# Kernel optimization log

Measured on AMD Instinct MI355X. Metric: run time of the kernel, lower is better.

## Reference

```python
import jax, jax.numpy as jnp
import numpy as np

EMBED = 1024
HIDDEN = 512
LN_EPS = 1e-5


def setup_inputs() -> dict:
    key = jax.random.key(0)
    ks = jax.random.split(key, 9)
    B, Sq, Skv = 4, 4096, 4096
    q_feat = jax.random.normal(ks[0], (B, Sq, EMBED), dtype=jnp.float32)
    kv_feat = jax.random.normal(ks[1], (B, Skv, EMBED), dtype=jnp.float32)
    # xavier-ish scale for weights; stored as [in, out]
    def w(k, fan_in, fan_out):
        s = (6.0 / (fan_in + fan_out)) ** 0.5
        return jax.random.uniform(k, (fan_in, fan_out), jnp.float32, -s, s)
    Wq = w(ks[2], EMBED, HIDDEN)
    Wk = w(ks[3], EMBED, HIDDEN)
    Wv = w(ks[4], EMBED, HIDDEN)
    Wo = w(ks[5], HIDDEN, EMBED)
    bo = jnp.zeros((EMBED,), jnp.float32)
    Wfc = w(ks[6], EMBED, EMBED)
    ln_gamma = jnp.ones((EMBED,), jnp.float32)
    ln_beta = jnp.zeros((EMBED,), jnp.float32)
    return {"q_feat": q_feat, "kv_feat": kv_feat, "Wq": Wq, "Wk": Wk, "Wv": Wv,
            "Wo": Wo, "bo": bo, "Wfc": Wfc, "ln_gamma": ln_gamma, "ln_beta": ln_beta}


def reference(q_feat, kv_feat, Wq, Wk, Wv, Wo, bo, Wfc, ln_gamma, ln_beta):
    # projections (single head)
    Q = jnp.einsum('bse,eh->bsh', q_feat, Wq)
    K = jnp.einsum('bse,eh->bsh', kv_feat, Wk)
    V = jnp.einsum('bse,eh->bsh', kv_feat, Wv)
    scale = 1.0 / jnp.sqrt(jnp.asarray(HIDDEN, Q.dtype))
    scores = jnp.einsum('bqh,bkh->bqk', Q, K) * scale  # [B, Sq, Skv]
    attn = jax.nn.softmax(scores, axis=-1)
    ctx = jnp.einsum('bqk,bkh->bqh', attn, V)
    out = jnp.einsum('bqh,he->bqe', ctx, Wo) + bo
    out = out + q_feat  # residual
    out = jnp.einsum('bqe,ef->bqf', out, Wfc)
    # layer norm over last dim
    mu = jnp.mean(out, axis=-1, keepdims=True)
    var = jnp.mean(jnp.square(out - mu), axis=-1, keepdims=True)
    out = (out - mu) * jax.lax.rsqrt(var + LN_EPS) * ln_gamma + ln_beta
    return out
```

## Files before the change

kernel.cpp:

```cpp
#include <hip/hip_runtime.h>
#include <hip/hip_bf16.h>
#include <cstdint>

typedef __bf16 bf16x8 __attribute__((ext_vector_type(8)));
typedef float f32x4 __attribute__((ext_vector_type(4)));
typedef unsigned short u16;
typedef unsigned short u16x8 __attribute__((ext_vector_type(8)));
typedef unsigned short u16x4 __attribute__((ext_vector_type(4)));

#define EMBED 1024
#define HIDDEN 512
#define SEQ 4096
#define NBATCH 4
#define MTOT (NBATCH * SEQ)
#define KVSPLIT 2

__device__ __forceinline__ u16 f32_to_bf16(float f) {
  union { float f; uint32_t u; } v; v.f = f;
  uint32_t r = v.u + 0x7fffu + ((v.u >> 16) & 1u);
  return (u16)(r >> 16);
}

__device__ __forceinline__ void load_lds16(const u16* g, u16* l) {
  __builtin_amdgcn_global_load_lds(
      (const __attribute__((address_space(1))) void*)g,
      (__attribute__((address_space(3))) void*)l, 16, 0, 0);
}

__global__ __launch_bounds__(256) void cvt_bf16_kernel(const float* __restrict__ src,
                                                       u16* __restrict__ dst) {
  int i = blockIdx.x * 256 + threadIdx.x;
  float4 v = ((const float4*)src)[i];
  u16x4 o;
  o[0] = f32_to_bf16(v.x); o[1] = f32_to_bf16(v.y);
  o[2] = f32_to_bf16(v.z); o[3] = f32_to_bf16(v.w);
  ((u16x4*)dst)[i] = o;
}

__global__ __launch_bounds__(256) void transpose_w_kernel(const float* __restrict__ src,
                                                          u16* __restrict__ dst,
                                                          int log2N, int K) {
  int idx = blockIdx.x * 256 + threadIdx.x;
  int N = 1 << log2N;
  int k = idx >> log2N;
  int n = idx & (N - 1);
  dst[(size_t)n * K + k] = f32_to_bf16(src[idx]);
}

template <int MODE>
__global__ __launch_bounds__(256, 3) void gemm_bt_kernel(
    const u16* __restrict__ A, const u16* __restrict__ Bt, void* __restrict__ Cout,
    const float* __restrict__ bias, const float* __restrict__ resid,
    int ldc, int K, float scale) {
  __shared__ u16 As[128][40];
  __shared__ u16 Bs[128][40];
  const int tid = threadIdx.x;
  const int lane = tid & 63;
  const int wave = tid >> 6;
  const int quad = lane >> 4;
  const int l15 = lane & 15;
  const int m0 = blockIdx.x * 128;
  const int n0 = blockIdx.y * 128;
  const int wm = (wave & 1) * 64;
  const int wn = (wave >> 1) * 64;

  f32x4 acc[4][4];
#pragma unroll
  for (int i = 0; i < 4; ++i)
#pragma unroll
    for (int j = 0; j < 4; ++j) {
      acc[i][j][0] = 0.f; acc[i][j][1] = 0.f; acc[i][j][2] = 0.f; acc[i][j][3] = 0.f;
    }

  for (int k0 = 0; k0 < K; k0 += 32) {
    __syncthreads();
#pragma unroll
    for (int p = 0; p < 2; ++p) {
      int c = tid + p * 256;
      int r = c >> 2;
      int c8 = (c & 3) * 8;
      *(u16x8*)&As[r][c8] = *(const u16x8*)&A[(size_t)(m0 + r) * K + k0 + c8];
      *(u16x8*)&Bs[r][c8] = *(const u16x8*)&Bt[(size_t)(n0 + r) * K + k0 + c8];
    }
    __syncthreads();
    bf16x8 af[4], bfr[4];
#pragma unroll
    for (int i = 0; i < 4; ++i) af[i] = *(const bf16x8*)&As[wm + i * 16 + l15][quad * 8];
#pragma unroll
    for (int j = 0; j < 4; ++j) bfr[j] = *(const bf16x8*)&Bs[wn + j * 16 + l15][quad * 8];
#pragma unroll
    for (int i = 0; i < 4; ++i)
#pragma unroll
      for (int j = 0; j < 4; ++j)
        acc[i][j] = __builtin_amdgcn_mfma_f32_16x16x32_bf16(af[i], bfr[j], acc[i][j], 0, 0, 0);
  }

#pragma unroll
  for (int i = 0; i < 4; ++i) {
    const int row = m0 + wm + i * 16 + quad * 4;
#pragma unroll
    for (int j = 0; j < 4; ++j) {
      const int col = n0 + wn + j * 16 + l15;
#pragma unroll
      for (int r = 0; r < 4; ++r) {
        float v = acc[i][j][r];
        const int rr = row + r;
        if (MODE == 0) {
          ((u16*)Cout)[(size_t)rr * ldc + col] = f32_to_bf16(v * scale);
        } else if (MODE == 1) {
          const size_t off = (size_t)rr * ldc + col;
          v += bias[col] + resid[off];
          ((u16*)Cout)[off] = f32_to_bf16(v);
        } else if (MODE == 2) {
          ((float*)Cout)[(size_t)rr * ldc + col] = v;
        } else {
          ((u16*)Cout)[((size_t)((rr >> 12) * 512 + col) << 12) + (rr & 4095)] = f32_to_bf16(v);
        }
      }
    }
  }
}

__global__ __launch_bounds__(256, 2) void flash_kernel(const u16* __restrict__ QKV,
                                                       const u16* __restrict__ VtG,
                                                       float* __restrict__ Opart,
                                                       float* __restrict__ ml) {
  __shared__ u16 Ks[32][520];
  __shared__ u16 Vs[512][32];
  __shared__ u16 Ps[4][16][40];
  const int tid = threadIdx.x;
  const int lane = tid & 63;
  const int wave = tid >> 6;
  const int quad = lane >> 4;
  const int l15 = lane & 15;
  const int base = blockIdx.y * SEQ;
  const int b512 = blockIdx.y * 512;
  const int q0 = blockIdx.x * 64;
  const int kvb = blockIdx.z * (SEQ / KVSPLIT);

  bf16x8 qf[16];
  {
    const u16* qp = QKV + (size_t)(base + q0 + wave * 16 + l15) * 1024 + quad * 8;
#pragma unroll
    for (int ks = 0; ks < 16; ++ks) qf[ks] = *(const bf16x8*)(qp + ks * 32);
  }

  f32x4 O[32];
#pragma unroll
  for (int i = 0; i < 32; ++i) { O[i][0] = 0.f; O[i][1] = 0.f; O[i][2] = 0.f; O[i][3] = 0.f; }
  float m_run[4] = {-INFINITY, -INFINITY, -INFINITY, -INFINITY};
  float l_run[4] = {0.f, 0.f, 0.f, 0.f};

  for (int kv0 = kvb; kv0 < kvb + SEQ / KVSPLIT; kv0 += 32) {
    __syncthreads();
    {
      const int rk = wave * 8;
      const u16* kp = QKV + (size_t)(base + kv0 + rk) * 1024 + 512 + lane * 8;
      const u16* vp = VtG + (size_t)(b512 + wave * 128 + (lane >> 2)) * 4096 + kv0 +
                      (((lane & 3) ^ ((lane >> 3) & 3)) * 8);
#pragma unroll
      for (int p = 0; p < 8; ++p) {
        load_lds16(kp + (size_t)p * 1024, &Ks[rk + p][0]);
        load_lds16(vp + (size_t)(p * 16) * 4096, &Vs[wave * 128 + p * 16][0]);
      }
    }
    __syncthreads();

    f32x4 s0, s1;
    s0[0] = 0.f; s0[1] = 0.f; s0[2] = 0.f; s0[3] = 0.f;
    s1[0] = 0.f; s1[1] = 0.f; s1[2] = 0.f; s1[3] = 0.f;
#pragma unroll
    for (int ks = 0; ks < 16; ++ks) {
      bf16x8 b0 = *(const bf16x8*)&Ks[l15][ks * 32 + quad * 8];
      bf16x8 b1 = *(const bf16x8*)&Ks[16 + l15][ks * 32 + quad * 8];
      s0 = __builtin_amdgcn_mfma_f32_16x16x32_bf16(qf[ks], b0, s0, 0, 0, 0);
      s1 = __builtin_amdgcn_mfma_f32_16x16x32_bf16(qf[ks], b1, s1, 0, 0, 0);
    }

    float tmax[4], alpha[4], p0[4], p1[4], tsum[4];
#pragma unroll
    for (int r = 0; r < 4; ++r) tmax[r] = fmaxf(s0[r], s1[r]);
#pragma unroll
    for (int m = 1; m <= 8; m <<= 1)
#pragma unroll
      for (int r = 0; r < 4; ++r) tmax[r] = fmaxf(tmax[r], __shfl_xor(tmax[r], m));
    bool aone = true;
#pragma unroll
    for (int r = 0; r < 4; ++r) {
      float mnew = fmaxf(m_run[r], tmax[r]);
      alpha[r] = __expf(m_run[r] - mnew);
      m_run[r] = mnew;
      p0[r] = __expf(s0[r] - mnew);
      p1[r] = __expf(s1[r] - mnew);
      tsum[r] = p0[r] + p1[r];
      aone = aone && (alpha[r] == 1.0f);
    }
#pragma unroll
    for (int m = 1; m <= 8; m <<= 1)
#pragma unroll
      for (int r = 0; r < 4; ++r) tsum[r] += __shfl_xor(tsum[r], m);
#pragma unroll
    for (int r = 0; r < 4; ++r) l_run[r] = l_run[r] * alpha[r] + tsum[r];
    if (!__all(aone)) {
#pragma unroll
      for (int i = 0; i < 32; ++i)
#pragma unroll
        for (int r = 0; r < 4; ++r) O[i][r] *= alpha[r];
    }

#pragma unroll
    for (int r = 0; r < 4; ++r) {
      Ps[wave][quad * 4 + r][l15] = f32_to_bf16(p0[r]);
      Ps[wave][quad * 4 + r][16 + l15] = f32_to_bf16(p1[r]);
    }
    asm volatile("s_waitcnt lgkmcnt(0)" ::: "memory");
    bf16x8 pf = *(const bf16x8*)&Ps[wave][l15][quad * 8];
#pragma unroll
    for (int nt = 0; nt < 32; ++nt) {
      bf16x8 vf = *(const bf16x8*)&Vs[nt * 16 + l15][(quad ^ ((l15 >> 1) & 3)) * 8];
      O[nt] = __builtin_amdgcn_mfma_f32_16x16x32_bf16(pf, vf, O[nt], 0, 0, 0);
    }
  }

  const int qrow = base + q0 + wave * 16 + quad * 4;
  float* op = Opart + ((size_t)blockIdx.z * MTOT + qrow) * HIDDEN;
#pragma unroll
  for (int nt = 0; nt < 32; ++nt)
#pragma unroll
    for (int r = 0; r < 4; ++r)
      op[(size_t)r * HIDDEN + nt * 16 + l15] = O[nt][r];
  if (l15 == 0) {
#pragma unroll
    for (int r = 0; r < 4; ++r) {
      ml[((size_t)blockIdx.z * MTOT + qrow + r) * 2 + 0] = m_run[r];
      ml[((size_t)blockIdx.z * MTOT + qrow + r) * 2 + 1] = l_run[r];
    }
  }
}

__global__ __launch_bounds__(128) void combine_kernel(const float* __restrict__ Op,
                                                      const float* __restrict__ ml,
                                                      u16* __restrict__ ctx) {
  const int row = blockIdx.x;
  const int tid = threadIdx.x;
  const float m1 = ml[(size_t)row * 2], l1 = ml[(size_t)row * 2 + 1];
  const float m2 = ml[((size_t)MTOT + row) * 2], l2 = ml[((size_t)MTOT + row) * 2 + 1];
  const float M = fmaxf(m1, m2);
  const float w1 = __expf(m1 - M), w2 = __expf(m2 - M);
  const float den = 1.0f / (w1 * l1 + w2 * l2);
  float4 a = ((const float4*)(Op + (size_t)row * HIDDEN))[tid];
  float4 b = ((const float4*)(Op + ((size_t)MTOT + row) * HIDDEN))[tid];
  u16x4 o;
  o[0] = f32_to_bf16((a.x * w1 + b.x * w2) * den);
  o[1] = f32_to_bf16((a.y * w1 + b.y * w2) * den);
  o[2] = f32_to_bf16((a.z * w1 + b.z * w2) * den);
  o[3] = f32_to_bf16((a.w * w1 + b.w * w2) * den);
  ((u16x4*)(ctx + (size_t)row * HIDDEN))[tid] = o;
}

__global__ __launch_bounds__(256) void ln_kernel(float* __restrict__ io,
                                                 const float* __restrict__ g,
                                                 const float* __restrict__ b) {
  const int row = blockIdx.x;
  const int tid = threadIdx.x;
  float* x = io + (size_t)row * EMBED;
  float4 v = *(const float4*)(x + tid * 4);
  float s1 = v.x + v.y + v.z + v.w;
  float s2 = v.x * v.x + v.y * v.y + v.z * v.z + v.w * v.w;
#pragma unroll
  for (int m = 1; m <= 32; m <<= 1) {
    s1 += __shfl_xor(s1, m);
    s2 += __shfl_xor(s2, m);
  }
  __shared__ float rs1[4], rs2[4];
  const int wave = tid >> 6;
  if ((tid & 63) == 0) { rs1[wave] = s1; rs2[wave] = s2; }
  __syncthreads();
  s1 = rs1[0] + rs1[1] + rs1[2] + rs1[3];
  s2 = rs2[0] + rs2[1] + rs2[2] + rs2[3];
  const float mu = s1 * (1.f / EMBED);
  const float var = s2 * (1.f / EMBED) - mu * mu;
  const float rinv = rsqrtf(var + 1e-5f);
  float4 gg = *(const float4*)(g + tid * 4);
  float4 bb = *(const float4*)(b + tid * 4);
  float4 o;
  o.x = (v.x - mu) * rinv * gg.x + bb.x;
  o.y = (v.y - mu) * rinv * gg.y + bb.y;
  o.z = (v.z - mu) * rinv * gg.z + bb.z;
  o.w = (v.w - mu) * rinv * gg.w + bb.w;
  *(float4*)(x + tid * 4) = o;
}

extern "C" void kernel_launch(void* const* d_in, const int* in_sizes, int n_in,
                              void* d_out, int out_size, void* d_ws, size_t ws_size,
                              hipStream_t stream) {
  const float* q_feat = (const float*)d_in[0];
  const float* kv_feat = (const float*)d_in[1];
  const float* Wq = (const float*)d_in[2];
  const float* Wk = (const float*)d_in[3];
  const float* Wv = (const float*)d_in[4];
  const float* Wo = (const float*)d_in[5];
  const float* bo = (const float*)d_in[6];
  const float* Wfc = (const float*)d_in[7];
  const float* ln_g = (const float*)d_in[8];
  const float* ln_b = (const float*)d_in[9];
  float* out = (float*)d_out;

  char* ws = (char*)d_ws;
  u16* Aq    = (u16*)(ws + 0);
  u16* Akv   = (u16*)(ws + 33554432);
  u16* Wcat  = (u16*)(ws + 67108864);
  u16* Wo_t  = (u16*)(ws + 70254592);
  u16* Wfc_t = (u16*)(ws + 71303168);
  u16* QKV   = (u16*)(ws + 73400320);
  u16* Vt    = (u16*)(ws + 106954752);
  u16* ctx   = (u16*)(ws + 123731968);
  u16* out1  = Aq;
  float* Opart = (float*)(ws + 0);
  float* mlp   = (float*)(ws + 67108864);

  const float qscale = 0.044194173824159216f;

  cvt_bf16_kernel<<<MTOT * EMBED / 1024, 256, 0, stream>>>(q_feat, Aq);
  cvt_bf16_kernel<<<MTOT * EMBED / 1024, 256, 0, stream>>>(kv_feat, Akv);
  transpose_w_kernel<<<(EMBED * HIDDEN) / 256, 256, 0, stream>>>(Wq, Wcat, 9, EMBED);
  transpose_w_kernel<<<(EMBED * HIDDEN) / 256, 256, 0, stream>>>(Wk, Wcat + 512 * 1024, 9, EMBED);
  transpose_w_kernel<<<(EMBED * HIDDEN) / 256, 256, 0, stream>>>(Wv, Wcat + 1024 * 1024, 9, EMBED);
  transpose_w_kernel<<<(HIDDEN * EMBED) / 256, 256, 0, stream>>>(Wo, Wo_t, 10, HIDDEN);
  transpose_w_kernel<<<(EMBED * EMBED) / 256, 256, 0, stream>>>(Wfc, Wfc_t, 10, EMBED);
  gemm_bt_kernel<0><<<dim3(MTOT / 128, 4), 256, 0, stream>>>(
      Aq, Wcat, QKV, nullptr, nullptr, 1024, EMBED, qscale);
  gemm_bt_kernel<0><<<dim3(MTOT / 128, 4), 256, 0, stream>>>(
      Akv, Wcat + 512 * 1024, QKV + 512, nullptr, nullptr, 1024, EMBED, 1.0f);
  gemm_bt_kernel<3><<<dim3(MTOT / 128, 4), 256, 0, stream>>>(
      Akv, Wcat + 1024 * 1024, Vt, nullptr, nullptr, 0, EMBED, 1.0f);
  flash_kernel<<<dim3(SEQ / 64, NBATCH, KVSPLIT), 256, 0, stream>>>(QKV, Vt, Opart, mlp);
  combine_kernel<<<MTOT, 128, 0, stream>>>(Opart, mlp, ctx);
  gemm_bt_kernel<1><<<dim3(MTOT / 128, EMBED / 128), 256, 0, stream>>>(
      ctx, Wo_t, out1, bo, q_feat, EMBED, HIDDEN, 0.f);
  gemm_bt_kernel<2><<<dim3(MTOT / 128, EMBED / 128), 256, 0, stream>>>(
      out1, Wfc_t, out, nullptr, nullptr, EMBED, EMBED, 0.f);
  ln_kernel<<<MTOT, 256, 0, stream>>>(out, ln_g, ln_b);

  (void)in_sizes; (void)n_in; (void)out_size; (void)ws_size;
}
```

Baseline: 672.5 us.

## Double-buffer K/V tiles in flash kernel with 128-row query blocks

Restructures the flash attention kernel to use 512-thread blocks covering 128 query rows, so each K/V tile loaded into LDS is shared by twice as many waves. K/V staging is double-buffered: the next tile is issued before computing on the current one, which removes one barrier per iteration. The block index is also remapped so consecutive blocks cover different batch and split pairs, and MFMA sections are raised with s_setprio. LDS use roughly doubles and the 512-thread launch bound with 2 blocks per CU tightens register limits, which risks spilling the 128-float O accumulator.

```diff
diff --git a/kernel.cpp b/kernel.cpp
--- a/kernel.cpp
+++ b/kernel.cpp
@@ -14,6 +14,7 @@
 #define NBATCH 4
 #define MTOT (NBATCH * SEQ)
 #define KVSPLIT 2
+#define QT 128
 
 __device__ __forceinline__ u16 f32_to_bf16(float f) {
   union { float f; uint32_t u; } v; v.f = f;
@@ -121,22 +122,27 @@
   }
 }
 
-__global__ __launch_bounds__(256, 2) void flash_kernel(const u16* __restrict__ QKV,
+__global__ __launch_bounds__(512, 2) void flash_kernel(const u16* __restrict__ QKV,
                                                        const u16* __restrict__ VtG,
                                                        float* __restrict__ Opart,
                                                        float* __restrict__ ml) {
-  __shared__ u16 Ks[32][520];
-  __shared__ u16 Vs[512][32];
-  __shared__ u16 Ps[4][16][40];
+  __shared__ u16 Ks[2][32][520];
+  __shared__ u16 Vs[2][512][32];
+  __shared__ u16 Ps[8][16][40];
   const int tid = threadIdx.x;
   const int lane = tid & 63;
   const int wave = tid >> 6;
   const int quad = lane >> 4;
   const int l15 = lane & 15;
-  const int base = blockIdx.y * SEQ;
-  const int b512 = blockIdx.y * 512;
-  const int q0 = blockIdx.x * 64;
-  const int kvb = blockIdx.z * (SEQ / KVSPLIT);
+  const int raw = blockIdx.x + 32 * blockIdx.y + 128 * blockIdx.z;
+  const int xh = raw >> 3;
+  const int g = raw & 7;
+  const int yh = g >> 1;
+  const int zh = g & 1;
+  const int base = yh * SEQ;
+  const int b512 = yh * 512;
+  const int q0 = xh * QT;
+  const int kvb = zh * (SEQ / KVSPLIT);
 
   bf16x8 qf[16];
   {
@@ -151,31 +157,38 @@
   float m_run[4] = {-INFINITY, -INFINITY, -INFINITY, -INFINITY};
   float l_run[4] = {0.f, 0.f, 0.f, 0.f};
 
-  for (int kv0 = kvb; kv0 < kvb + SEQ / KVSPLIT; kv0 += 32) {
-    __syncthreads();
-    {
-      const int rk = wave * 8;
-      const u16* kp = QKV + (size_t)(base + kv0 + rk) * 1024 + 512 + lane * 8;
-      const u16* vp = VtG + (size_t)(b512 + wave * 128 + (lane >> 2)) * 4096 + kv0 +
-                      (((lane & 3) ^ ((lane >> 3) & 3)) * 8);
-#pragma unroll
-      for (int p = 0; p < 8; ++p) {
-        load_lds16(kp + (size_t)p * 1024, &Ks[rk + p][0]);
-        load_lds16(vp + (size_t)(p * 16) * 4096, &Vs[wave * 128 + p * 16][0]);
-      }
-    }
-    __syncthreads();
+  auto STAGE = [&](int b, int kv0) {
+    const u16* kp = QKV + (size_t)(base + kv0 + wave * 4) * 1024 + 512 + lane * 8;
+    const u16* vp = VtG + (size_t)(b512 + wave * 64 + (lane >> 2)) * 4096 + kv0 +
+                    (((lane & 3) ^ ((lane >> 3) & 3)) * 8);
+#pragma unroll
+    for (int p = 0; p < 4; ++p) {
+      load_lds16(kp + (size_t)p * 1024, &Ks[b][wave * 4 + p][0]);
+      load_lds16(vp + (size_t)(p * 16) * 4096, &Vs[b][wave * 64 + p * 16][0]);
+    }
+  };
+
+  const int nIter = (SEQ / KVSPLIT) / 32;
+  STAGE(0, kvb);
+  asm volatile("s_waitcnt vmcnt(0)" ::: "memory");
+  __builtin_amdgcn_s_barrier();
+  int cur = 0;
+
+  for (int t = 0; t < nIter; ++t) {
+    if (t + 1 < nIter) STAGE(cur ^ 1, kvb + (t + 1) * 32);
 
     f32x4 s0, s1;
     s0[0] = 0.f; s0[1] = 0.f; s0[2] = 0.f; s0[3] = 0.f;
     s1[0] = 0.f; s1[1] = 0.f; s1[2] = 0.f; s1[3] = 0.f;
+    __builtin_amdgcn_s_setprio(1);
 #pragma unroll
     for (int ks = 0; ks < 16; ++ks) {
-      bf16x8 b0 = *(const bf16x8*)&Ks[l15][ks * 32 + quad * 8];
-      bf16x8 b1 = *(const bf16x8*)&Ks[16 + l15][ks * 32 + quad * 8];
+      bf16x8 b0 = *(const bf16x8*)&Ks[cur][l15][ks * 32 + quad * 8];
+      bf16x8 b1 = *(const bf16x8*)&Ks[cur][16 + l15][ks * 32 + quad * 8];
       s0 = __builtin_amdgcn_mfma_f32_16x16x32_bf16(qf[ks], b0, s0, 0, 0, 0);
       s1 = __builtin_amdgcn_mfma_f32_16x16x32_bf16(qf[ks], b1, s1, 0, 0, 0);
     }
+    __builtin_amdgcn_s_setprio(0);
 
     float tmax[4], alpha[4], p0[4], p1[4], tsum[4];
 #pragma unroll
@@ -215,15 +228,21 @@
     }
     asm volatile("s_waitcnt lgkmcnt(0)" ::: "memory");
     bf16x8 pf = *(const bf16x8*)&Ps[wave][l15][quad * 8];
+    __builtin_amdgcn_s_setprio(1);
 #pragma unroll
     for (int nt = 0; nt < 32; ++nt) {
-      bf16x8 vf = *(const bf16x8*)&Vs[nt * 16 + l15][(quad ^ ((l15 >> 1) & 3)) * 8];
+      bf16x8 vf = *(const bf16x8*)&Vs[cur][nt * 16 + l15][(quad ^ ((l15 >> 1) & 3)) * 8];
       O[nt] = __builtin_amdgcn_mfma_f32_16x16x32_bf16(pf, vf, O[nt], 0, 0, 0);
     }
+    __builtin_amdgcn_s_setprio(0);
+
+    asm volatile("s_waitcnt vmcnt(0)" ::: "memory");
+    __builtin_amdgcn_s_barrier();
+    cur ^= 1;
   }
 
   const int qrow = base + q0 + wave * 16 + quad * 4;
-  float* op = Opart + ((size_t)blockIdx.z * MTOT + qrow) * HIDDEN;
+  float* op = Opart + ((size_t)zh * MTOT + qrow) * HIDDEN;
 #pragma unroll
   for (int nt = 0; nt < 32; ++nt)
 #pragma unroll
@@ -232,8 +251,8 @@
   if (l15 == 0) {
 #pragma unroll
     for (int r = 0; r < 4; ++r) {
-      ml[((size_t)blockIdx.z * MTOT + qrow + r) * 2 + 0] = m_run[r];
-      ml[((size_t)blockIdx.z * MTOT + qrow + r) * 2 + 1] = l_run[r];
+      ml[((size_t)zh * MTOT + qrow + r) * 2 + 0] = m_run[r];
+      ml[((size_t)zh * MTOT + qrow + r) * 2 + 1] = l_run[r];
     }
   }
 }
@@ -334,7 +353,7 @@
       Akv, Wcat + 512 * 1024, QKV + 512, nullptr, nullptr, 1024, EMBED, 1.0f);
   gemm_bt_kernel<3><<<dim3(MTOT / 128, 4), 256, 0, stream>>>(
       Akv, Wcat + 1024 * 1024, Vt, nullptr, nullptr, 0, EMBED, 1.0f);
-  flash_kernel<<<dim3(SEQ / 64, NBATCH, KVSPLIT), 256, 0, stream>>>(QKV, Vt, Opart, mlp);
+  flash_kernel<<<dim3(SEQ / QT, NBATCH, KVSPLIT), 512, 0, stream>>>(QKV, Vt, Opart, mlp);
   combine_kernel<<<MTOT, 128, 0, stream>>>(Opart, mlp, ctx);
   gemm_bt_kernel<1><<<dim3(MTOT / 128, EMBED / 128), 256, 0, stream>>>(
       ctx, Wo_t, out1, bo, q_feat, EMBED, HIDDEN, 0.f);
```

After: 656.7 us. 2.4% less time.
